# Kernel optimization log

Hardware: AMD Instinct MI355X
Metric: run time of the kernel (lower is better)

## Reference

```python
import jax, jax.numpy as jnp
import numpy as np

N_NODES = 20000
N_EDGES = 320000  # directed edges, in reverse pairs (2*i, 2*i+1)
F_NODE = 64
F_EDGE = 16
HID = 300
DEPTH = 3
N_GRAPHS = 128


def setup_inputs() -> dict:
    key = jax.random.key(0)
    ks = jax.random.split(key, 16)
    x = jax.random.normal(ks[0], (N_NODES, F_NODE), dtype=jnp.float32)
    edge_attr = jax.random.normal(ks[1], (N_EDGES, F_EDGE), dtype=jnp.float32)
    # build paired directed edges: edge 2*i is (src,dst), edge 2*i+1 is (dst,src)
    half = N_EDGES // 2
    src = jax.random.randint(ks[2], (half,), 0, N_NODES)
    dst = jax.random.randint(ks[3], (half,), 0, N_NODES)
    row = jnp.stack([src, dst], axis=1).reshape(-1)  # [E]
    col = jnp.stack([dst, src], axis=1).reshape(-1)  # [E]
    edge_index = jnp.stack([row, col], axis=0)  # [2, E]
    batch = jnp.sort(jax.random.randint(ks[4], (N_NODES,), 0, N_GRAPHS))
    s = 0.05
    W_init = jax.random.normal(ks[5], (F_NODE + F_EDGE, HID), dtype=jnp.float32) * s
    b_init = jnp.zeros((HID,), dtype=jnp.float32)
    W_convs = jax.random.normal(ks[6], (DEPTH, HID, HID), dtype=jnp.float32) * s
    b_convs = jnp.zeros((DEPTH, HID), dtype=jnp.float32)
    W_e2n = jax.random.normal(ks[7], (F_NODE + HID, HID), dtype=jnp.float32) * s
    b_e2n = jnp.zeros((HID,), dtype=jnp.float32)
    W_ffn = jax.random.normal(ks[8], (HID, 1), dtype=jnp.float32) * s
    b_ffn = jnp.zeros((1,), dtype=jnp.float32)
    return {"x": x, "edge_attr": edge_attr, "edge_index": edge_index, "batch": batch,
            "W_init": W_init, "b_init": b_init, "W_convs": W_convs, "b_convs": b_convs,
            "W_e2n": W_e2n, "b_e2n": b_e2n, "W_ffn": W_ffn, "b_ffn": b_ffn}


def _rev(h):
    # swap each consecutive forward/reverse edge pair
    e = h.shape[0]
    return h.reshape(e // 2, 2, -1)[:, ::-1, :].reshape(e, -1)


def reference(x, edge_attr, edge_index, batch, W_init, b_init, W_convs, b_convs,
              W_e2n, b_e2n, W_ffn, b_ffn):
    row, col = edge_index[0], edge_index[1]
    # h_0 = act(edge_init(cat([x[row], edge_attr])))
    h0 = jax.nn.relu(jnp.concatenate([x[row], edge_attr], axis=1) @ W_init + b_init)
    h = h0
    for l in range(DEPTH):
        # DMPNNConv: scatter-add edge features to target nodes, gather at source,
        # subtract reverse-edge message, apply Linear
        a = jax.ops.segment_sum(h, col, num_segments=N_NODES)  # [N, H]
        h = (a[row] - _rev(h)) @ W_convs[l] + b_convs[l]
        h = jax.nn.relu(h + h0)  # skip then activation; dropout is eval no-op
    # final conv's a_message only
    s = jax.ops.segment_sum(h, col, num_segments=N_NODES)  # [N, H]
    q = jnp.concatenate([x, s], axis=1)
    hn = jax.nn.relu(q @ W_e2n + b_e2n)  # [N, H]
    pooled = jax.ops.segment_sum(hn, batch, num_segments=N_GRAPHS)  # [G, H]
    return (pooled @ W_ffn + b_ffn).squeeze(-1)  # [G]
```

## Files before the change

kernel.cpp:

```cpp
#include <hip/hip_runtime.h>
#include <hip/hip_bf16.h>

typedef unsigned short ushort_t;
typedef __attribute__((ext_vector_type(8))) short short8;
typedef __attribute__((ext_vector_type(4))) float f32x4;
typedef __attribute__((ext_vector_type(2))) float f32x2;

#define N_NODES 20000
#define N_EDGES 320000
#define F_NODE 64
#define F_EDGE 16
#define HID 300
#define HP 300
#define NTILES 20
#define DEPTH 3
#define N_GRAPHS 128
#define KE2N 384
#define ATS 328

#define WFRAG_USHORT_PER_LAYER (10 * NTILES * 64 * 8)
#define W2FRAG_USHORT (NTILES * 64 * 8)
#define WE2NFRAG_USHORT (12 * NTILES * 64 * 8)

__device__ __forceinline__ float bf2f(ushort_t u) {
    union { unsigned int i; float f; } v;
    v.i = ((unsigned int)u) << 16;
    return v.f;
}

__device__ __forceinline__ f32x2 bfpair(unsigned int u) {
    union { unsigned int i[2]; f32x2 f; } v;
    v.i[0] = u << 16;
    v.i[1] = u & 0xffff0000u;
    return v.f;
}

__device__ __forceinline__ f32x2 pmax0(f32x2 a) {
#if __has_builtin(__builtin_elementwise_max)
    f32x2 z = {0.f, 0.f};
    return __builtin_elementwise_max(a, z);
#else
    f32x2 r; r.x = fmaxf(a.x, 0.f); r.y = fmaxf(a.y, 0.f); return r;
#endif
}

__device__ __forceinline__ unsigned int fpack(float lo, float hi) {
#if __has_builtin(__builtin_amdgcn_cvt_pk_bf16_f32)
    auto r = __builtin_amdgcn_cvt_pk_bf16_f32(lo, hi);
    union { decltype(r) b; unsigned int u; } v;
    v.b = r;
    return v.u;
#else
    union { float f; unsigned int i; } a, b;
    a.f = lo; b.f = hi;
    return ((a.i + 0x8000u) >> 16) | ((b.i + 0x8000u) & 0xffff0000u);
#endif
}
__device__ __forceinline__ unsigned int fpack2(f32x2 a) { return fpack(a.x, a.y); }
__device__ __forceinline__ ushort_t f2bf(float f) {
    return (ushort_t)(fpack(f, 0.f) & 0xffffu);
}

__global__ __launch_bounds__(256) void csr_hist(
    const int* __restrict__ col, int* __restrict__ deg)
{
    int e = blockIdx.x * 256 + threadIdx.x;
    atomicAdd(&deg[col[e]], 1);
}

__global__ __launch_bounds__(256) void csr_scan(
    const int* __restrict__ deg, int* __restrict__ offsets,
    int* __restrict__ cursor)
{
    __shared__ int sums[256];
    const int t = threadIdx.x;
    const int CH = 79;
    int base = t * CH;
    int local = 0;
    for (int i = 0; i < CH; ++i) {
        int idx = base + i;
        if (idx < N_NODES) local += deg[idx];
    }
    sums[t] = local;
    __syncthreads();
    for (int off = 1; off < 256; off <<= 1) {
        int v = (t >= off) ? sums[t - off] : 0;
        __syncthreads();
        sums[t] += v;
        __syncthreads();
    }
    int run = (t > 0) ? sums[t - 1] : 0;
    for (int i = 0; i < CH; ++i) {
        int idx = base + i;
        if (idx < N_NODES) {
            offsets[idx] = run;
            cursor[idx] = run;
            run += deg[idx];
        }
    }
}

__global__ __launch_bounds__(256) void csr_fill(
    const int* __restrict__ col, int* __restrict__ cursor,
    int* __restrict__ eid)
{
    int e = blockIdx.x * 256 + threadIdx.x;
    int pos = atomicAdd(&cursor[col[e]], 1);
    eid[pos] = e;
}

__global__ __launch_bounds__(256) void ghist(
    const int* __restrict__ batch, int* __restrict__ gdeg)
{
    int n = blockIdx.x * 256 + threadIdx.x;
    if (n < N_NODES) atomicAdd(&gdeg[batch[n]], 1);
}

__global__ __launch_bounds__(128) void gscan(
    const int* __restrict__ gdeg, int* __restrict__ goff)
{
    __shared__ int s[128];
    int t = threadIdx.x;
    int d = gdeg[t];
    s[t] = d;
    __syncthreads();
    for (int off = 1; off < 128; off <<= 1) {
        int v = (t >= off) ? s[t - off] : 0;
        __syncthreads();
        s[t] += v;
        __syncthreads();
    }
    goff[t] = s[t] - d;
    if (t == 127) goff[128] = s[127];
}

__global__ __launch_bounds__(64) void wfrag_build(
    const float* __restrict__ W_convs, ushort_t* __restrict__ wfrag)
{
    const int c = blockIdx.x, t = blockIdx.y, l = blockIdx.z;
    const int lane = threadIdx.x;
    const int k0 = c * 32 + (lane >> 4) * 8;
    const int n  = t * 16 + (lane & 15);
    ushort_t* dst = wfrag + (size_t)l * WFRAG_USHORT_PER_LAYER
                  + ((size_t)(c * NTILES + t) * 64 + lane) * 8;
    const float* Wl = W_convs + (size_t)l * HID * HID;
    #pragma unroll
    for (int j = 0; j < 8; ++j) {
        int k = k0 + j;
        float v = (k < HID && n < HID) ? Wl[(long)k * HID + n] : 0.f;
        dst[j] = f2bf(v);
    }
}

__global__ __launch_bounds__(64) void wfrag2_build(
    const float* __restrict__ W_e2n, ushort_t* __restrict__ wfrag2)
{
    const int c = blockIdx.x, t = blockIdx.y;
    const int lane = threadIdx.x;
    const int k0 = c * 32 + (lane >> 4) * 8;
    const int n  = t * 16 + (lane & 15);
    ushort_t* dst = wfrag2 + ((size_t)(c * NTILES + t) * 64 + lane) * 8;
    #pragma unroll
    for (int j = 0; j < 8; ++j) {
        int k = k0 + j;
        float v = (k < F_NODE + HID && n < HID) ? W_e2n[(long)k * HID + n] : 0.f;
        dst[j] = f2bf(v);
    }
}

__global__ __launch_bounds__(64) void w2frag_build(
    const float* __restrict__ W2, ushort_t* __restrict__ w2frag)
{
    const int t = blockIdx.x;
    const int lane = threadIdx.x;
    const int k0 = (lane >> 4) * 8;
    const int n  = t * 16 + (lane & 15);
    ushort_t* dst = w2frag + ((size_t)t * 64 + lane) * 8;
    #pragma unroll
    for (int j = 0; j < 8; ++j) {
        int k = k0 + j;
        float v = (k < F_EDGE && n < HID) ? W2[(long)k * HID + n] : 0.f;
        dst[j] = f2bf(v);
    }
}


__global__ __launch_bounds__(256) void node_init_gemm(
    const float* __restrict__ x, const float* __restrict__ W_init,
    const float* __restrict__ b_init, ushort_t* __restrict__ xW1b)
{
    __shared__ float xs[16 * 64];
    const int tid = threadIdx.x;
    const long n0 = (long)blockIdx.x * 16;
    for (int i = tid; i < 16 * 64; i += 256) xs[i] = x[n0 * 64 + i];
    __syncthreads();
    const int nl = tid >> 4, ct = tid & 15;
    for (int q = 0; q < 19; ++q) {
        int c = ct + 16 * q;
        if (c < HID) {
            float acc = b_init[c];
            #pragma unroll 8
            for (int k = 0; k < 64; ++k)
                acc = fmaf(xs[nl * 64 + k], W_init[(long)k * HID + c], acc);
            xW1b[(n0 + nl) * HID + c] = f2bf(acc);
        }
    }
}

__device__ __forceinline__ void p_phase8(
    ushort_t* At, const float* __restrict__ edge_attr,
    const ushort_t* __restrict__ w2frag, long e0,
    int wave, int quad, int m, int lane)
{
    const int mtp = wave >> 2;
    const int nt0p = (wave & 3) * 5;
    short8 a_ea;
    {
        union { uint4 u4; short8 s8; } af;
        if (quad < 2) {
            const float* eap = edge_attr + (e0 + mtp * 16 + m) * 16 + quad * 8;
            float4 v0 = *(const float4*)eap;
            float4 v1 = *(const float4*)(eap + 4);
            af.u4.x = fpack(v0.x, v0.y); af.u4.y = fpack(v0.z, v0.w);
            af.u4.z = fpack(v1.x, v1.y); af.u4.w = fpack(v1.z, v1.w);
        } else {
            af.u4.x = 0; af.u4.y = 0; af.u4.z = 0; af.u4.w = 0;
        }
        a_ea = af.s8;
    }
    #pragma unroll
    for (int t = 0; t < 5; ++t) {
        int nt = nt0p + t;
        if (nt >= 19) continue;
        short8 b = *(const short8*)(w2frag + ((size_t)nt * 64 + lane) * 8);
        int c = nt * 16 + m;
        f32x4 pc = (f32x4){0.f, 0.f, 0.f, 0.f};
        pc = __builtin_amdgcn_mfma_f32_16x16x32_bf16(a_ea, b, pc, 0, 0, 0);
        #pragma unroll
        for (int r = 0; r < 4; ++r)
            At[(mtp * 16 + quad * 4 + r) * ATS + c] = f2bf(pc[r]);
    }
}

template<bool UPDATE>
__global__ __launch_bounds__(256) void fused_conv(
    ushort_t* h, const ushort_t* __restrict__ Sb,
    const ushort_t* __restrict__ xW1b, const float* __restrict__ edge_attr,
    const int* __restrict__ row, const ushort_t* __restrict__ w2frag,
    const ushort_t* __restrict__ wfrag_l)
{
    __shared__ ushort_t At[32 * ATS];
    const int tid = threadIdx.x;
    const int wave = tid >> 6, lane = tid & 63;
    const int quad = lane >> 4, m = lane & 15;
    const long e0 = (long)blockIdx.x * 32;

    auto issue = [&](int k, uint2& xa, uint2& xb, uint2& wa, uint2& wb,
                     uint2& sa, uint2& sb, int& la, int& lb, int& g) {
        int i = tid + (k << 8);
        int p = i / 80; g = i % 80;
        la = 2 * p; lb = la + 1;
        if (g < 75) {
            int c0 = 4 * g;
            int ra = row[e0 + la], rb = row[e0 + lb];
            xa = *(const uint2*)&xW1b[(long)ra * HID + c0];
            xb = *(const uint2*)&xW1b[(long)rb * HID + c0];
            if (UPDATE) {
                wa = *(const uint2*)&h[(e0 + la) * HP + c0];
                wb = *(const uint2*)&h[(e0 + lb) * HP + c0];
                sa = *(const uint2*)&Sb[(long)ra * HID + c0];
                sb = *(const uint2*)&Sb[(long)rb * HID + c0];
            }
        }
    };

    uint2 xa0, xb0, wa0, wb0, sa0, sb0;
    int la0, lb0, g0;
    issue(0, xa0, xb0, wa0, wb0, sa0, sb0, la0, lb0, g0);

    {
        short8 a_ea[2];
        #pragma unroll
        for (int mt = 0; mt < 2; ++mt) {
            union { uint4 u4; short8 s8; } af;
            if (quad < 2) {
                const float* eap = edge_attr + (e0 + mt * 16 + m) * 16 + quad * 8;
                float4 v0 = *(const float4*)eap;
                float4 v1 = *(const float4*)(eap + 4);
                af.u4.x = fpack(v0.x, v0.y); af.u4.y = fpack(v0.z, v0.w);
                af.u4.z = fpack(v1.x, v1.y); af.u4.w = fpack(v1.z, v1.w);
            } else {
                af.u4.x = 0; af.u4.y = 0; af.u4.z = 0; af.u4.w = 0;
            }
            a_ea[mt] = af.s8;
        }
        const int nt0 = wave * 5;
        #pragma unroll
        for (int t = 0; t < 5; ++t) {
            short8 b = *(const short8*)(w2frag + ((size_t)(nt0 + t) * 64 + lane) * 8);
            int c = (nt0 + t) * 16 + m;
            #pragma unroll
            for (int mt = 0; mt < 2; ++mt) {
                f32x4 pc = (f32x4){0.f, 0.f, 0.f, 0.f};
                pc = __builtin_amdgcn_mfma_f32_16x16x32_bf16(a_ea[mt], b, pc, 0, 0, 0);
                #pragma unroll
                for (int r = 0; r < 4; ++r)
                    At[(mt * 16 + quad * 4 + r) * ATS + c] = f2bf(pc[r]);
            }
        }
    }
    __syncthreads();

    #pragma unroll
    for (int k = 0; k < 5; ++k) {
        uint2 xa1, xb1, wa1, wb1, sa1, sb1;
        int la1 = 0, lb1 = 0, g1 = 0;
        if (k < 4)
            issue(k + 1, xa1, xb1, wa1, wb1, sa1, sb1, la1, lb1, g1);
        int c0 = 4 * g0;
        uint2 oa, ob;
        if (g0 < 75) {
            uint2 pa = *(const uint2*)&At[la0 * ATS + c0];
            uint2 pb = *(const uint2*)&At[lb0 * ATS + c0];
            f32x2 h0a0 = pmax0(bfpair(xa0.x) + bfpair(pa.x));
            f32x2 h0a1 = pmax0(bfpair(xa0.y) + bfpair(pa.y));
            f32x2 h0b0 = pmax0(bfpair(xb0.x) + bfpair(pb.x));
            f32x2 h0b1 = pmax0(bfpair(xb0.y) + bfpair(pb.y));
            if (UPDATE) {
                oa.x = fpack2(pmax0(bfpair(sa0.x) - bfpair(wb0.x) + h0a0));
                oa.y = fpack2(pmax0(bfpair(sa0.y) - bfpair(wb0.y) + h0a1));
                ob.x = fpack2(pmax0(bfpair(sb0.x) - bfpair(wa0.x) + h0b0));
                ob.y = fpack2(pmax0(bfpair(sb0.y) - bfpair(wa0.y) + h0b1));
            } else {
                oa.x = fpack2(h0a0); oa.y = fpack2(h0a1);
                ob.x = fpack2(h0b0); ob.y = fpack2(h0b1);
            }
        } else {
            oa.x = 0; oa.y = 0;
            ob = oa;
        }
        *(uint2*)&At[la0 * ATS + c0] = oa;
        *(uint2*)&At[lb0 * ATS + c0] = ob;
        if (k < 4) {
            xa0 = xa1; xb0 = xb1; wa0 = wa1; wb0 = wb1;
            sa0 = sa1; sb0 = sb1; la0 = la1; lb0 = lb1; g0 = g1;
        }
    }
    __syncthreads();

    const int nt0 = wave * 5;
    f32x4 acc[5][2];
    #pragma unroll
    for (int t = 0; t < 5; ++t)
        #pragma unroll
        for (int mt = 0; mt < 2; ++mt)
            acc[t][mt] = (f32x4){0.f, 0.f, 0.f, 0.f};

    short8 bc[5], ac[2];
    #pragma unroll
    for (int t = 0; t < 5; ++t)
        bc[t] = *(const short8*)(wfrag_l + ((size_t)(nt0 + t) * 64 + lane) * 8);
    #pragma unroll
    for (int mt = 0; mt < 2; ++mt)
        ac[mt] = *(const short8*)&At[(mt * 16 + m) * ATS + quad * 8];

    #pragma unroll
    for (int c = 0; c < 10; ++c) {
        short8 bn[5], an[2];
        if (c < 9) {
            #pragma unroll
            for (int t = 0; t < 5; ++t)
                bn[t] = *(const short8*)(wfrag_l
                    + ((size_t)((c + 1) * NTILES + nt0 + t) * 64 + lane) * 8);
            #pragma unroll
            for (int mt = 0; mt < 2; ++mt)
                an[mt] = *(const short8*)&At[(mt * 16 + m) * ATS
                    + (c + 1) * 32 + quad * 8];
        }
        #pragma unroll
        for (int t = 0; t < 5; ++t)
            #pragma unroll
            for (int mt = 0; mt < 2; ++mt)
                acc[t][mt] = __builtin_amdgcn_mfma_f32_16x16x32_bf16(
                    ac[mt], bc[t], acc[t][mt], 0, 0, 0);
        if (c < 9) {
            #pragma unroll
            for (int t = 0; t < 5; ++t) bc[t] = bn[t];
            ac[0] = an[0]; ac[1] = an[1];
        }
    }
    #pragma unroll
    for (int t = 0; t < 5; ++t) {
        int col = (nt0 + t) * 16 + m;
        if (col >= HID) continue;
        #pragma unroll
        for (int mt = 0; mt < 2; ++mt) {
            long rbase = (e0 + mt * 16 + quad * 4) * HP + col;
            #pragma unroll
            for (int r = 0; r < 4; ++r)
                h[rbase + (long)r * HP] = f2bf(acc[t][mt][r]);
        }
    }
}

__global__ __launch_bounds__(512) void edge_update_mfma(
    ushort_t* h, const ushort_t* __restrict__ Sb,
    const ushort_t* __restrict__ xW1b, const float* __restrict__ edge_attr,
    const int* __restrict__ row, const ushort_t* __restrict__ w2frag)
{
    __shared__ ushort_t Pt[32 * ATS];
    const int tid = threadIdx.x;
    const int wave = tid >> 6, lane = tid & 63;
    const int quad = lane >> 4, m = lane & 15;
    const long e0 = (long)blockIdx.x * 32;

    auto issue = [&](int k, uint2& xa, uint2& xb, uint2& wa, uint2& wb,
                     uint2& sa, uint2& sb, int& la, int& lb, int& g, bool& v) {
        int i = tid + (k << 9);
        v = i < 16 * 75;
        if (v) {
            int p = i / 75; g = i % 75;
            la = 2 * p; lb = la + 1;
            int c0 = 4 * g;
            int ra = row[e0 + la], rb = row[e0 + lb];
            xa = *(const uint2*)&xW1b[(long)ra * HID + c0];
            xb = *(const uint2*)&xW1b[(long)rb * HID + c0];
            wa = *(const uint2*)&h[(e0 + la) * HP + c0];
            wb = *(const uint2*)&h[(e0 + lb) * HP + c0];
            sa = *(const uint2*)&Sb[(long)ra * HID + c0];
            sb = *(const uint2*)&Sb[(long)rb * HID + c0];
        }
    };

    uint2 xa0, xb0, wa0, wb0, sa0, sb0;
    int la0 = 0, lb0 = 0, g0 = 0; bool v0 = false;
    issue(0, xa0, xb0, wa0, wb0, sa0, sb0, la0, lb0, g0, v0);

    p_phase8(Pt, edge_attr, w2frag, e0, wave, quad, m, lane);
    __syncthreads();

    #pragma unroll
    for (int k = 0; k < 3; ++k) {
        uint2 xa1, xb1, wa1, wb1, sa1, sb1;
        int la1 = 0, lb1 = 0, g1 = 0; bool v1 = false;
        if (k < 2)
            issue(k + 1, xa1, xb1, wa1, wb1, sa1, sb1, la1, lb1, g1, v1);
        if (v0) {
            int c0 = 4 * g0;
            uint2 pa = *(const uint2*)&Pt[la0 * ATS + c0];
            uint2 pb = *(const uint2*)&Pt[lb0 * ATS + c0];
            f32x2 h0a0 = pmax0(bfpair(xa0.x) + bfpair(pa.x));
            f32x2 h0a1 = pmax0(bfpair(xa0.y) + bfpair(pa.y));
            f32x2 h0b0 = pmax0(bfpair(xb0.x) + bfpair(pb.x));
            f32x2 h0b1 = pmax0(bfpair(xb0.y) + bfpair(pb.y));
            uint2 oa, ob;
            oa.x = fpack2(pmax0(bfpair(sa0.x) - bfpair(wb0.x) + h0a0));
            oa.y = fpack2(pmax0(bfpair(sa0.y) - bfpair(wb0.y) + h0a1));
            ob.x = fpack2(pmax0(bfpair(sb0.x) - bfpair(wa0.x) + h0b0));
            ob.y = fpack2(pmax0(bfpair(sb0.y) - bfpair(wa0.y) + h0b1));
            *(uint2*)&h[(e0 + la0) * HP + c0] = oa;
            *(uint2*)&h[(e0 + lb0) * HP + c0] = ob;
        }
        if (k < 2) {
            xa0 = xa1; xb0 = xb1; wa0 = wa1; wb0 = wb1;
            sa0 = sa1; sb0 = sb1; la0 = la1; lb0 = lb1; g0 = g1; v0 = v1;
        }
    }
}

__global__ __launch_bounds__(256) void gather_sum(
    const ushort_t* __restrict__ src, const int* __restrict__ offsets,
    const int* __restrict__ ends, const int* __restrict__ eid,
    const float* __restrict__ bias, ushort_t* __restrict__ Sb)
{
    long idx = (long)blockIdx.x * 256 + threadIdx.x;
    if (idx >= (long)N_NODES * 75) return;
    int n = (int)(idx / 75);
    int g = (int)(idx % 75);
    int beg = offsets[n], end = ends[n];
    f32x2 A0 = {0.f, 0.f}, A1 = {0.f, 0.f};
    f32x2 B0 = {0.f, 0.f}, B1 = {0.f, 0.f};
    f32x2 C0 = {0.f, 0.f}, C1 = {0.f, 0.f};
    f32x2 D0 = {0.f, 0.f}, D1 = {0.f, 0.f};
    int j = beg;
    for (; j + 3 < end; j += 4) {
        int ea = eid[j], eb = eid[j + 1], ec = eid[j + 2], ed = eid[j + 3];
        uint2 va = ((const uint2*)src)[(long)ea * (HP / 4) + g];
        uint2 vb = ((const uint2*)src)[(long)eb * (HP / 4) + g];
        uint2 vc = ((const uint2*)src)[(long)ec * (HP / 4) + g];
        uint2 vd = ((const uint2*)src)[(long)ed * (HP / 4) + g];
        A0 += bfpair(va.x); A1 += bfpair(va.y);
        B0 += bfpair(vb.x); B1 += bfpair(vb.y);
        C0 += bfpair(vc.x); C1 += bfpair(vc.y);
        D0 += bfpair(vd.x); D1 += bfpair(vd.y);
    }
    for (; j < end; ++j) {
        int ea = eid[j];
        uint2 va = ((const uint2*)src)[(long)ea * (HP / 4) + g];
        A0 += bfpair(va.x); A1 += bfpair(va.y);
    }
    float4 bv = *(const float4*)&bias[4 * g];
    f32x2 bv0 = {bv.x, bv.y}, bv1 = {bv.z, bv.w};
    uint2 o;
    o.x = fpack2((A0 + B0) + (C0 + D0) + bv0);
    o.y = fpack2((A1 + B1) + (C1 + D1) + bv1);
    *(uint2*)&Sb[(long)n * HID + 4 * g] = o;
}

__global__ __launch_bounds__(256) void gather_ab(
    const ushort_t* __restrict__ src, const int* __restrict__ offsets,
    const int* __restrict__ ends, const int* __restrict__ eid,
    ushort_t* __restrict__ Ab)
{
    long idx = (long)blockIdx.x * 256 + threadIdx.x;
    if (idx >= (long)N_NODES * 75) return;
    int n = (int)(idx / 75);
    int g = (int)(idx % 75);
    int beg = offsets[n], end = ends[n];
    f32x2 A0 = {0.f, 0.f}, A1 = {0.f, 0.f};
    f32x2 B0 = {0.f, 0.f}, B1 = {0.f, 0.f};
    f32x2 C0 = {0.f, 0.f}, C1 = {0.f, 0.f};
    f32x2 D0 = {0.f, 0.f}, D1 = {0.f, 0.f};
    int j = beg;
    for (; j + 3 < end; j += 4) {
        int ea = eid[j], eb = eid[j + 1], ec = eid[j + 2], ed = eid[j + 3];
        uint2 va = ((const uint2*)src)[(long)ea * (HP / 4) + g];
        uint2 vb = ((const uint2*)src)[(long)eb * (HP / 4) + g];
        uint2 vc = ((const uint2*)src)[(long)ec * (HP / 4) + g];
        uint2 vd = ((const uint2*)src)[(long)ed * (HP / 4) + g];
        A0 += bfpair(va.x); A1 += bfpair(va.y);
        B0 += bfpair(vb.x); B1 += bfpair(vb.y);
        C0 += bfpair(vc.x); C1 += bfpair(vc.y);
        D0 += bfpair(vd.x); D1 += bfpair(vd.y);
    }
    for (; j < end; ++j) {
        int ea = eid[j];
        uint2 va = ((const uint2*)src)[(long)ea * (HP / 4) + g];
        A0 += bfpair(va.x); A1 += bfpair(va.y);
    }
    uint2 o;
    o.x = fpack2((A0 + B0) + (C0 + D0));
    o.y = fpack2((A1 + B1) + (C1 + D1));
    *(uint2*)&Ab[(long)n * KE2N + 64 + 4 * g] = o;
}

__global__ __launch_bounds__(256) void x_fill(
    const float* __restrict__ x, ushort_t* __restrict__ Ab)
{
    long idx = (long)blockIdx.x * 256 + threadIdx.x;
    if (idx >= (long)N_NODES * 21) return;
    int n = (int)(idx / 21);
    int q = (int)(idx % 21);
    if (q < 16) {
        float4 v = *(const float4*)&x[(long)n * 64 + 4 * q];
        uint2 o;
        o.x = fpack(v.x, v.y);
        o.y = fpack(v.z, v.w);
        *(uint2*)&Ab[(long)n * KE2N + 4 * q] = o;
    } else {
        uint2 o; o.x = 0; o.y = 0;
        *(uint2*)&Ab[(long)n * KE2N + 364 + 4 * (q - 16)] = o;
    }
}

__global__ __launch_bounds__(256) void e2n_mfma(
    const ushort_t* __restrict__ Ab, const ushort_t* __restrict__ wfrag2,
    const float* __restrict__ b_e2n, float* __restrict__ hn)
{
    const int tid = threadIdx.x;
    const int wave = tid >> 6, lane = tid & 63;
    const int quad = lane >> 4, m = lane & 15;
    const long n0 = (long)blockIdx.x * 64;
    const int nt0 = wave * 5;

    f32x4 acc[5][4];
    #pragma unroll
    for (int t = 0; t < 5; ++t)
        #pragma unroll
        for (int mt = 0; mt < 4; ++mt)
            acc[t][mt] = (f32x4){0.f, 0.f, 0.f, 0.f};

    for (int c = 0; c < 12; ++c) {
        short8 a[4];
        #pragma unroll
        for (int mt = 0; mt < 4; ++mt) {
            long r = n0 + mt * 16 + m;
            if (r > N_NODES - 1) r = N_NODES - 1;
            a[mt] = *(const short8*)(Ab + r * KE2N + c * 32 + quad * 8);
        }
        #pragma unroll
        for (int t = 0; t < 5; ++t) {
            short8 b = *(const short8*)(wfrag2
                + ((size_t)(c * NTILES + nt0 + t) * 64 + lane) * 8);
            #pragma unroll
            for (int mt = 0; mt < 4; ++mt)
                acc[t][mt] = __builtin_amdgcn_mfma_f32_16x16x32_bf16(
                    a[mt], b, acc[t][mt], 0, 0, 0);
        }
    }

    #pragma unroll
    for (int t = 0; t < 5; ++t) {
        int col = (nt0 + t) * 16 + m;
        if (col >= HID) continue;
        float bias = b_e2n[col];
        #pragma unroll
        for (int mt = 0; mt < 4; ++mt) {
            long rw = n0 + mt * 16 + quad * 4;
            #pragma unroll
            for (int r = 0; r < 4; ++r) {
                long rowi = rw + r;
                if (rowi < N_NODES)
                    hn[rowi * HP + col] = fmaxf(acc[t][mt][r] + bias, 0.f);
            }
        }
    }
}

__global__ __launch_bounds__(256) void pool_graph(
    const float* __restrict__ hn, const int* __restrict__ goff,
    float* __restrict__ pooled)
{
    int g = blockIdx.x;
    int beg = goff[g], end = goff[g + 1];
    for (int c = threadIdx.x; c < HID; c += 256) {
        float acc = 0.f;
        for (int n = beg; n < end; ++n)
            acc += hn[(long)n * HP + c];
        pooled[(long)g * HID + c] = acc;
    }
}

__global__ __launch_bounds__(64) void ffn_out(
    const float* __restrict__ pooled, const float* __restrict__ W_ffn,
    const float* __restrict__ b_ffn, float* __restrict__ out)
{
    int g = blockIdx.x;
    int lane = threadIdx.x;
    float s = 0.f;
    for (int c = lane; c < HID; c += 64)
        s += pooled[(long)g * HID + c] * W_ffn[c];
    #pragma unroll
    for (int off = 32; off > 0; off >>= 1)
        s += __shfl_down(s, off, 64);
    if (lane == 0) out[g] = s + b_ffn[0];
}

extern "C" void kernel_launch(void* const* d_in, const int* in_sizes, int n_in,
                              void* d_out, int out_size, void* d_ws, size_t ws_size,
                              hipStream_t stream) {
    const float* x         = (const float*)d_in[0];
    const float* edge_attr = (const float*)d_in[1];
    const int*   edge_index= (const int*)d_in[2];
    const int*   batch     = (const int*)d_in[3];
    const float* W_init    = (const float*)d_in[4];
    const float* b_init    = (const float*)d_in[5];
    const float* W_convs   = (const float*)d_in[6];
    const float* b_convs   = (const float*)d_in[7];
    const float* W_e2n     = (const float*)d_in[8];
    const float* b_e2n     = (const float*)d_in[9];
    const float* W_ffn     = (const float*)d_in[10];
    const float* b_ffn     = (const float*)d_in[11];
    float* out = (float*)d_out;

    const int* row = edge_index;
    const int* col = edge_index + N_EDGES;
    const float* W2 = W_init + (size_t)F_NODE * HID;

    const size_t need = (size_t)N_EDGES * HP * 2
                      + (size_t)N_NODES * HID * 2
                      + (size_t)N_NODES * KE2N * 2
                      + (size_t)N_GRAPHS * HID * 4
                      + (size_t)N_NODES * 4 * 2 + (size_t)N_EDGES * 4
                      + (size_t)DEPTH * WFRAG_USHORT_PER_LAYER * 2
                      + (size_t)WE2NFRAG_USHORT * 2
                      + (size_t)W2FRAG_USHORT * 2
                      + (size_t)(N_GRAPHS + 1 + N_GRAPHS) * 4 + 32768;
    if (ws_size < need) return;

    char* p = (char*)d_ws;
    auto take = [&](size_t bytes) {
        char* q = p;
        p += (bytes + 255) & ~(size_t)255;
        return q;
    };
    ushort_t* h       = (ushort_t*)take((size_t)N_EDGES * HP * 2);
    ushort_t* Sb      = (ushort_t*)take((size_t)N_NODES * HID * 2);
    ushort_t* Ab      = (ushort_t*)take((size_t)N_NODES * KE2N * 2);
    float*    pooled  = (float*)take((size_t)N_GRAPHS * HID * 4);
    int*      cursor  = (int*)take((size_t)N_NODES * 4);
    int*      offsets = (int*)take((size_t)N_NODES * 4);
    int*      eid     = (int*)take((size_t)N_EDGES * 4);
    ushort_t* wfrag   = (ushort_t*)take((size_t)DEPTH * WFRAG_USHORT_PER_LAYER * 2);
    ushort_t* wfrag2  = (ushort_t*)take((size_t)WE2NFRAG_USHORT * 2);
    ushort_t* w2frag  = (ushort_t*)take((size_t)W2FRAG_USHORT * 2);
    int*      gdeg    = (int*)take((size_t)N_GRAPHS * 4);
    int*      goff    = (int*)take((size_t)(N_GRAPHS + 1) * 4);

    ushort_t* xW1b = Ab;
    float*    hn   = (float*)h;

    hipMemsetAsync(cursor, 0, (size_t)N_NODES * 4, stream);
    hipMemsetAsync(gdeg, 0, (size_t)N_GRAPHS * 4, stream);
    csr_hist<<<N_EDGES / 256, 256, 0, stream>>>(col, cursor);
    csr_scan<<<1, 256, 0, stream>>>(cursor, offsets, cursor);
    csr_fill<<<N_EDGES / 256, 256, 0, stream>>>(col, cursor, eid);
    ghist<<<(N_NODES + 255) / 256, 256, 0, stream>>>(batch, gdeg);
    gscan<<<1, 128, 0, stream>>>(gdeg, goff);

    wfrag_build<<<dim3(10, NTILES, DEPTH), 64, 0, stream>>>(W_convs, wfrag);
    wfrag2_build<<<dim3(12, NTILES, 1), 64, 0, stream>>>(W_e2n, wfrag2);
    w2frag_build<<<NTILES, 64, 0, stream>>>(W2, w2frag);

    node_init_gemm<<<N_NODES / 16, 256, 0, stream>>>(x, W_init, b_init, xW1b);

    const int GS_GRID = ((N_NODES * 75) + 255) / 256;

    fused_conv<false><<<N_EDGES / 32, 256, 0, stream>>>(
        h, Sb, xW1b, edge_attr, row, w2frag, wfrag);
    gather_sum<<<GS_GRID, 256, 0, stream>>>(
        h, offsets, cursor, eid, b_convs + 0 * HID, Sb);
    fused_conv<true><<<N_EDGES / 32, 256, 0, stream>>>(
        h, Sb, xW1b, edge_attr, row, w2frag,
        wfrag + 1 * (size_t)WFRAG_USHORT_PER_LAYER);
    gather_sum<<<GS_GRID, 256, 0, stream>>>(
        h, offsets, cursor, eid, b_convs + 1 * HID, Sb);
    fused_conv<true><<<N_EDGES / 32, 256, 0, stream>>>(
        h, Sb, xW1b, edge_attr, row, w2frag,
        wfrag + 2 * (size_t)WFRAG_USHORT_PER_LAYER);
    gather_sum<<<GS_GRID, 256, 0, stream>>>(
        h, offsets, cursor, eid, b_convs + 2 * HID, Sb);
    edge_update_mfma<<<N_EDGES / 32, 512, 0, stream>>>(
        h, Sb, xW1b, edge_attr, row, w2frag);

    x_fill<<<((N_NODES * 21) + 255) / 256, 256, 0, stream>>>(x, Ab);
    gather_ab<<<GS_GRID, 256, 0, stream>>>(h, offsets, cursor, eid, Ab);
    e2n_mfma<<<(N_NODES + 63) / 64, 256, 0, stream>>>(Ab, wfrag2, b_e2n, hn);
    pool_graph<<<N_GRAPHS, 256, 0, stream>>>(hn, goff, pooled);
    ffn_out<<<N_GRAPHS, 64, 0, stream>>>(pooled, W_ffn, b_ffn, out);
}
```

Baseline: 1.285 ms.

## Simplify fused_conv loads, pad LDS stride, and halve e2n tile rows

Removes the software-pipelined register prefetch of gathered xW1b/h/Sb rows and of the MFMA weight and LDS fragments in fused_conv, replacing them with a plain loop that loads each element on use. Row indices are now staged once in shared memory. The LDS row stride grows from 328 to 344 to change the bank mapping. e2n_mfma now processes 32 nodes per block instead of 64, giving more blocks and dropping the bounds clamps because 20000 divides by 32. The change trades explicit latency hiding for lower register pressure and possibly higher occupancy, and relies on the compiler and the hardware to hide latency.

Measured after the change: 1.211 ms. -5.8%, faster.

```diff
diff --git a/kernel.cpp b/kernel.cpp
--- a/kernel.cpp
+++ b/kernel.cpp
@@ -16,7 +16,7 @@
 #define DEPTH 3
 #define N_GRAPHS 128
 #define KE2N 384
-#define ATS 328
+#define ATS 344
 
 #define WFRAG_USHORT_PER_LAYER (10 * NTILES * 64 * 8)
 #define W2FRAG_USHORT (NTILES * 64 * 8)
@@ -250,33 +250,12 @@
     const ushort_t* __restrict__ wfrag_l)
 {
     __shared__ ushort_t At[32 * ATS];
+    __shared__ int rows[32];
     const int tid = threadIdx.x;
     const int wave = tid >> 6, lane = tid & 63;
     const int quad = lane >> 4, m = lane & 15;
     const long e0 = (long)blockIdx.x * 32;
-
-    auto issue = [&](int k, uint2& xa, uint2& xb, uint2& wa, uint2& wb,
-                     uint2& sa, uint2& sb, int& la, int& lb, int& g) {
-        int i = tid + (k << 8);
-        int p = i / 80; g = i % 80;
-        la = 2 * p; lb = la + 1;
-        if (g < 75) {
-            int c0 = 4 * g;
-            int ra = row[e0 + la], rb = row[e0 + lb];
-            xa = *(const uint2*)&xW1b[(long)ra * HID + c0];
-            xb = *(const uint2*)&xW1b[(long)rb * HID + c0];
-            if (UPDATE) {
-                wa = *(const uint2*)&h[(e0 + la) * HP + c0];
-                wb = *(const uint2*)&h[(e0 + lb) * HP + c0];
-                sa = *(const uint2*)&Sb[(long)ra * HID + c0];
-                sb = *(const uint2*)&Sb[(long)rb * HID + c0];
-            }
-        }
-    };
-
-    uint2 xa0, xb0, wa0, wb0, sa0, sb0;
-    int la0, lb0, g0;
-    issue(0, xa0, xb0, wa0, wb0, sa0, sb0, la0, lb0, g0);
+    if (tid < 32) rows[tid] = row[e0 + tid];
 
     {
         short8 a_ea[2];
@@ -311,26 +290,31 @@
     }
     __syncthreads();
 
-    #pragma unroll
-    for (int k = 0; k < 5; ++k) {
-        uint2 xa1, xb1, wa1, wb1, sa1, sb1;
-        int la1 = 0, lb1 = 0, g1 = 0;
-        if (k < 4)
-            issue(k + 1, xa1, xb1, wa1, wb1, sa1, sb1, la1, lb1, g1);
-        int c0 = 4 * g0;
+    for (int i = tid; i < 16 * 80; i += 256) {
+        int p = i / 80, g = i % 80;
+        int c0 = 4 * g;
+        int la = 2 * p, lb = 2 * p + 1;
         uint2 oa, ob;
-        if (g0 < 75) {
-            uint2 pa = *(const uint2*)&At[la0 * ATS + c0];
-            uint2 pb = *(const uint2*)&At[lb0 * ATS + c0];
-            f32x2 h0a0 = pmax0(bfpair(xa0.x) + bfpair(pa.x));
-            f32x2 h0a1 = pmax0(bfpair(xa0.y) + bfpair(pa.y));
-            f32x2 h0b0 = pmax0(bfpair(xb0.x) + bfpair(pb.x));
-            f32x2 h0b1 = pmax0(bfpair(xb0.y) + bfpair(pb.y));
+        if (g < 75) {
+            long Ea = e0 + la, Eb = e0 + lb;
+            int ra = rows[la], rb = rows[lb];
+            uint2 xa = *(const uint2*)&xW1b[(long)ra * HID + c0];
+            uint2 xb = *(const uint2*)&xW1b[(long)rb * HID + c0];
+            uint2 pa = *(const uint2*)&At[la * ATS + c0];
+            uint2 pb = *(const uint2*)&At[lb * ATS + c0];
+            f32x2 h0a0 = pmax0(bfpair(xa.x) + bfpair(pa.x));
+            f32x2 h0a1 = pmax0(bfpair(xa.y) + bfpair(pa.y));
+            f32x2 h0b0 = pmax0(bfpair(xb.x) + bfpair(pb.x));
+            f32x2 h0b1 = pmax0(bfpair(xb.y) + bfpair(pb.y));
             if (UPDATE) {
-                oa.x = fpack2(pmax0(bfpair(sa0.x) - bfpair(wb0.x) + h0a0));
-                oa.y = fpack2(pmax0(bfpair(sa0.y) - bfpair(wb0.y) + h0a1));
-                ob.x = fpack2(pmax0(bfpair(sb0.x) - bfpair(wa0.x) + h0b0));
-                ob.y = fpack2(pmax0(bfpair(sb0.y) - bfpair(wa0.y) + h0b1));
+                uint2 wa = *(const uint2*)&h[Ea * HP + c0];
+                uint2 wb = *(const uint2*)&h[Eb * HP + c0];
+                uint2 sa = *(const uint2*)&Sb[(long)ra * HID + c0];
+                uint2 sb = *(const uint2*)&Sb[(long)rb * HID + c0];
+                oa.x = fpack2(pmax0(bfpair(sa.x) - bfpair(wb.x) + h0a0));
+                oa.y = fpack2(pmax0(bfpair(sa.y) - bfpair(wb.y) + h0a1));
+                ob.x = fpack2(pmax0(bfpair(sb.x) - bfpair(wa.x) + h0b0));
+                ob.y = fpack2(pmax0(bfpair(sb.y) - bfpair(wa.y) + h0b1));
             } else {
                 oa.x = fpack2(h0a0); oa.y = fpack2(h0a1);
                 ob.x = fpack2(h0b0); ob.y = fpack2(h0b1);
@@ -339,12 +323,8 @@
             oa.x = 0; oa.y = 0;
             ob = oa;
         }
-        *(uint2*)&At[la0 * ATS + c0] = oa;
-        *(uint2*)&At[lb0 * ATS + c0] = ob;
-        if (k < 4) {
-            xa0 = xa1; xb0 = xb1; wa0 = wa1; wb0 = wb1;
-            sa0 = sa1; sb0 = sb1; la0 = la1; lb0 = lb1; g0 = g1;
-        }
+        *(uint2*)&At[la * ATS + c0] = oa;
+        *(uint2*)&At[lb * ATS + c0] = ob;
     }
     __syncthreads();
 
@@ -356,37 +336,19 @@
         for (int mt = 0; mt < 2; ++mt)
             acc[t][mt] = (f32x4){0.f, 0.f, 0.f, 0.f};
 
-    short8 bc[5], ac[2];
-    #pragma unroll
-    for (int t = 0; t < 5; ++t)
-        bc[t] = *(const short8*)(wfrag_l + ((size_t)(nt0 + t) * 64 + lane) * 8);
-    #pragma unroll
-    for (int mt = 0; mt < 2; ++mt)
-        ac[mt] = *(const short8*)&At[(mt * 16 + m) * ATS + quad * 8];
-
-    #pragma unroll
     for (int c = 0; c < 10; ++c) {
-        short8 bn[5], an[2];
-        if (c < 9) {
-            #pragma unroll
-            for (int t = 0; t < 5; ++t)
-                bn[t] = *(const short8*)(wfrag_l
-                    + ((size_t)((c + 1) * NTILES + nt0 + t) * 64 + lane) * 8);
-            #pragma unroll
-            for (int mt = 0; mt < 2; ++mt)
-                an[mt] = *(const short8*)&At[(mt * 16 + m) * ATS
-                    + (c + 1) * 32 + quad * 8];
-        }
-        #pragma unroll
-        for (int t = 0; t < 5; ++t)
+        short8 a[2];
+        #pragma unroll
+        for (int mt = 0; mt < 2; ++mt)
+            a[mt] = *(const short8*)&At[(mt * 16 + m) * ATS + c * 32 + quad * 8];
+        #pragma unroll
+        for (int t = 0; t < 5; ++t) {
+            short8 b = *(const short8*)(wfrag_l
+                + ((size_t)(c * NTILES + nt0 + t) * 64 + lane) * 8);
             #pragma unroll
             for (int mt = 0; mt < 2; ++mt)
                 acc[t][mt] = __builtin_amdgcn_mfma_f32_16x16x32_bf16(
-                    ac[mt], bc[t], acc[t][mt], 0, 0, 0);
-        if (c < 9) {
-            #pragma unroll
-            for (int t = 0; t < 5; ++t) bc[t] = bn[t];
-            ac[0] = an[0]; ac[1] = an[1];
+                    a[mt], b, acc[t][mt], 0, 0, 0);
         }
     }
     #pragma unroll
@@ -570,22 +532,21 @@
     const int tid = threadIdx.x;
     const int wave = tid >> 6, lane = tid & 63;
     const int quad = lane >> 4, m = lane & 15;
-    const long n0 = (long)blockIdx.x * 64;
+    const long n0 = (long)blockIdx.x * 32;
     const int nt0 = wave * 5;
 
-    f32x4 acc[5][4];
+    f32x4 acc[5][2];
     #pragma unroll
     for (int t = 0; t < 5; ++t)
         #pragma unroll
-        for (int mt = 0; mt < 4; ++mt)
+        for (int mt = 0; mt < 2; ++mt)
             acc[t][mt] = (f32x4){0.f, 0.f, 0.f, 0.f};
 
     for (int c = 0; c < 12; ++c) {
-        short8 a[4];
-        #pragma unroll
-        for (int mt = 0; mt < 4; ++mt) {
+        short8 a[2];
+        #pragma unroll
+        for (int mt = 0; mt < 2; ++mt) {
             long r = n0 + mt * 16 + m;
-            if (r > N_NODES - 1) r = N_NODES - 1;
             a[mt] = *(const short8*)(Ab + r * KE2N + c * 32 + quad * 8);
         }
         #pragma unroll
@@ -593,7 +554,7 @@
             short8 b = *(const short8*)(wfrag2
                 + ((size_t)(c * NTILES + nt0 + t) * 64 + lane) * 8);
             #pragma unroll
-            for (int mt = 0; mt < 4; ++mt)
+            for (int mt = 0; mt < 2; ++mt)
                 acc[t][mt] = __builtin_amdgcn_mfma_f32_16x16x32_bf16(
                     a[mt], b, acc[t][mt], 0, 0, 0);
         }
@@ -605,14 +566,11 @@
         if (col >= HID) continue;
         float bias = b_e2n[col];
         #pragma unroll
-        for (int mt = 0; mt < 4; ++mt) {
+        for (int mt = 0; mt < 2; ++mt) {
             long rw = n0 + mt * 16 + quad * 4;
             #pragma unroll
-            for (int r = 0; r < 4; ++r) {
-                long rowi = rw + r;
-                if (rowi < N_NODES)
-                    hn[rowi * HP + col] = fmaxf(acc[t][mt][r] + bias, 0.f);
-            }
+            for (int r = 0; r < 4; ++r)
+                hn[(rw + r) * HP + col] = fmaxf(acc[t][mt][r] + bias, 0.f);
         }
     }
 }
@@ -735,7 +693,7 @@
 
     x_fill<<<((N_NODES * 21) + 255) / 256, 256, 0, stream>>>(x, Ab);
     gather_ab<<<GS_GRID, 256, 0, stream>>>(h, offsets, cursor, eid, Ab);
-    e2n_mfma<<<(N_NODES + 63) / 64, 256, 0, stream>>>(Ab, wfrag2, b_e2n, hn);
+    e2n_mfma<<<N_NODES / 32, 256, 0, stream>>>(Ab, wfrag2, b_e2n, hn);
     pool_graph<<<N_GRAPHS, 256, 0, stream>>>(hn, goff, pooled);
     ffn_out<<<N_GRAPHS, 64, 0, stream>>>(pooled, W_ffn, b_ffn, out);
 }
```
